# Kernel optimization log

Measured on AMD Instinct MI355X. Metric: run time of the kernel, lower is better.

## Reference

```python
import jax, jax.numpy as jnp
import numpy as np

NUM_POINTS = 2_000_000
NUM_CAMS = 200
H, W = 1080, 1920


def setup_inputs() -> dict:
    key = jax.random.key(0)
    k1, k2, k3, k4, k5, k6, k7 = jax.random.split(key, 7)
    c = jax.random.randint(k1, (NUM_POINTS,), 0, NUM_CAMS)
    y = jax.random.randint(k2, (NUM_POINTS,), 0, H)
    x = jax.random.randint(k3, (NUM_POINTS,), 0, W)
    point_indices = jnp.stack([c, y, x], axis=1)  # [N,3] int
    depth = jax.random.uniform(k4, (NUM_POINTS, 1), minval=0.1, maxval=10.0, dtype=jnp.float32)
    # nerfstudio get_image_coords(): pixel-center grid (row+0.5, col+0.5), shape [H,W,2]
    yy, xx = jnp.meshgrid(jnp.arange(H), jnp.arange(W), indexing='ij')
    image_coords = jnp.stack([yy, xx], axis=-1).astype(jnp.float32) + 0.5
    # camera_to_worlds: [C,3,4] = [R | t] with proper rotation (invertible when padded)
    Q, _ = jnp.linalg.qr(jax.random.normal(k5, (NUM_CAMS, 3, 3), dtype=jnp.float32))
    t = jax.random.normal(k6, (NUM_CAMS, 3, 1), dtype=jnp.float32) * 2.0
    camera_to_worlds = jnp.concatenate([Q, t], axis=-1)  # [C,3,4]
    # intrinsics: [C,3,3] pinhole matrices
    f = 1000.0 + 50.0 * jax.random.normal(k7, (NUM_CAMS,), dtype=jnp.float32)
    zeros = jnp.zeros_like(f)
    ones = jnp.ones_like(f)
    cx = jnp.full_like(f, W / 2.0)
    cy = jnp.full_like(f, H / 2.0)
    intrinsics = jnp.stack([
        jnp.stack([f, zeros, cx], axis=-1),
        jnp.stack([zeros, f, cy], axis=-1),
        jnp.stack([zeros, zeros, ones], axis=-1),
    ], axis=1)  # [C,3,3]
    return {
        'point_indices': point_indices,
        'depth': depth,
        'image_coords': image_coords,
        'camera_to_worlds': camera_to_worlds,
        'intrinsics': intrinsics,
    }


def reference(point_indices, depth, image_coords, camera_to_worlds, intrinsics):
    # camera_calib == 'xyz' -> no output axis permutation
    c = point_indices[:, 0]
    y = point_indices[:, 1]
    x = point_indices[:, 2]
    coords = image_coords[y, x] - 0.5  # [N,2] (row, col)
    d = depth  # [N,1]
    # X_img = [x*d, y*d, d, 1]
    X_img = jnp.concatenate([coords[:, [1, 0]] * d, d, jnp.ones_like(d)], axis=1)  # [N,4]
    # N2R = diag(1,-1,-1,1)
    n2r = jnp.diag(jnp.array([1.0, -1.0, -1.0, 1.0], dtype=jnp.float32))  # [4,4]
    E = camera_to_worlds[c]  # [N,3,4]
    bottom = jnp.broadcast_to(jnp.array([0.0, 0.0, 0.0, 1.0], dtype=jnp.float32), (E.shape[0], 1, 4))
    E_ = jnp.concatenate([E, bottom], axis=1)  # [N,4,4]
    K = intrinsics[c]  # [N,3,3]
    K_ = jnp.pad(K, ((0, 0), (0, 1), (0, 1)))  # [N,4,4] zero-padded
    K_ = K_.at[:, 3, 3].set(1.0)
    w2c = K_ @ jnp.linalg.inv(E_ @ n2r)  # [N,4,4]
    c2w = jnp.linalg.inv(w2c)
    X_world = (c2w @ X_img[..., None])[..., 0]  # [N,4]
    return X_world
```

## Files before the change

kernel.cpp:

```cpp
#include <hip/hip_runtime.h>


#define MAXCAM 256

__global__ __launch_bounds__(256) void pointgen_kernel(
    const int*   __restrict__ pi,
    const float* __restrict__ depth,
    const float* __restrict__ c2w,
    const float* __restrict__ intr,
    float4*      __restrict__ out,
    int N, int ncam)
{
    __shared__ float4 camA[MAXCAM * 3];

    for (int cam = (int)threadIdx.x; cam < ncam; cam += (int)blockDim.x) {
        const float* e = c2w  + cam * 12;
        const float* k = intr + cam * 9;
        float f  = k[0];
        float cx = k[2];
        float cy = k[5];
        float invf = 1.0f / f;
        #pragma unroll
        for (int r = 0; r < 3; ++r) {
            float R0 = e[r * 4 + 0];
            float R1 = e[r * 4 + 1];
            float R2 = e[r * 4 + 2];
            float tr = e[r * 4 + 3];
            float4 a;
            a.x = R0 * invf;
            a.y = -R1 * invf;
            a.z = (cy * R1 - cx * R0) * invf - R2;
            a.w = tr;
            camA[cam * 3 + r] = a;
        }
    }
    __syncthreads();

    int stride = (int)(gridDim.x * blockDim.x);
    for (int i = (int)(blockIdx.x * blockDim.x + threadIdx.x); i < N; i += stride) {
        int c = pi[3 * i + 0];
        int y = pi[3 * i + 1];
        int x = pi[3 * i + 2];
        float d = depth[i];
        float xd = (float)x * d;
        float yd = (float)y * d;
        float4 r0 = camA[c * 3 + 0];
        float4 r1 = camA[c * 3 + 1];
        float4 r2 = camA[c * 3 + 2];
        float4 o;
        o.x = fmaf(r0.x, xd, fmaf(r0.y, yd, fmaf(r0.z, d, r0.w)));
        o.y = fmaf(r1.x, xd, fmaf(r1.y, yd, fmaf(r1.z, d, r1.w)));
        o.z = fmaf(r2.x, xd, fmaf(r2.y, yd, fmaf(r2.z, d, r2.w)));
        o.w = 1.0f;
        out[i] = o;
    }
}

extern "C" void kernel_launch(void* const* d_in, const int* in_sizes, int n_in,
                              void* d_out, int out_size, void* d_ws, size_t ws_size,
                              hipStream_t stream) {
    const int*   pi    = (const int*)d_in[0];
    const float* depth = (const float*)d_in[1];
    const float* c2w   = (const float*)d_in[3];
    const float* intr  = (const float*)d_in[4];
    float4* out = (float4*)d_out;

    int N    = in_sizes[1];
    int ncam = in_sizes[3] / 12;
    if (ncam > MAXCAM) ncam = MAXCAM;

    int block = 256;
    int grid  = 1024;
    int max_grid = (N + block - 1) / block;
    if (grid > max_grid) grid = max_grid;

    pointgen_kernel<<<grid, block, 0, stream>>>(pi, depth, c2w, intr, out, N, ncam);
}
```

Before: 96.74 us.

## Process four points per thread with vectorized int4/float4 loads

Each thread now handles four consecutive points, reading the packed [N,3] indices as three int4 loads and the depths as one float4 load in place of scalar strided loads. The grid-stride loop is dropped for a one-shot grid sized to N/4 threads. The goal is fewer, wider memory transactions on a bandwidth-bound kernel. The cost is about 2000 blocks that each rebuild the 200-camera shared-memory table, versus 1024 before, and the wide loads assume the input buffers are 16-byte aligned.

```diff
diff --git a/kernel.cpp b/kernel.cpp
--- a/kernel.cpp
+++ b/kernel.cpp
@@ -3,7 +3,22 @@
 
 #define MAXCAM 256
 
-__global__ __launch_bounds__(256) void pointgen_kernel(
+__device__ __forceinline__ float4 proj(const float4* __restrict__ camA,
+                                       int c, int y, int x, float d) {
+    float xd = (float)x * d;
+    float yd = (float)y * d;
+    float4 r0 = camA[c * 3 + 0];
+    float4 r1 = camA[c * 3 + 1];
+    float4 r2 = camA[c * 3 + 2];
+    float4 o;
+    o.x = fmaf(r0.x, xd, fmaf(r0.y, yd, fmaf(r0.z, d, r0.w)));
+    o.y = fmaf(r1.x, xd, fmaf(r1.y, yd, fmaf(r1.z, d, r1.w)));
+    o.z = fmaf(r2.x, xd, fmaf(r2.y, yd, fmaf(r2.z, d, r2.w)));
+    o.w = 1.0f;
+    return o;
+}
+
+__global__ __launch_bounds__(256) void pointgen4_kernel(
     const int*   __restrict__ pi,
     const float* __restrict__ depth,
     const float* __restrict__ c2w,
@@ -36,23 +51,31 @@
     }
     __syncthreads();
 
-    int stride = (int)(gridDim.x * blockDim.x);
-    for (int i = (int)(blockIdx.x * blockDim.x + threadIdx.x); i < N; i += stride) {
-        int c = pi[3 * i + 0];
-        int y = pi[3 * i + 1];
-        int x = pi[3 * i + 2];
-        float d = depth[i];
-        float xd = (float)x * d;
-        float yd = (float)y * d;
-        float4 r0 = camA[c * 3 + 0];
-        float4 r1 = camA[c * 3 + 1];
-        float4 r2 = camA[c * 3 + 2];
-        float4 o;
-        o.x = fmaf(r0.x, xd, fmaf(r0.y, yd, fmaf(r0.z, d, r0.w)));
-        o.y = fmaf(r1.x, xd, fmaf(r1.y, yd, fmaf(r1.z, d, r1.w)));
-        o.z = fmaf(r2.x, xd, fmaf(r2.y, yd, fmaf(r2.z, d, r2.w)));
-        o.w = 1.0f;
-        out[i] = o;
+    int t    = (int)(blockIdx.x * blockDim.x + threadIdx.x);
+    int base = 4 * t;
+    if (base + 3 < N) {
+        const int4* pi4 = (const int4*)pi;
+        int4 w0 = pi4[3 * t + 0];
+        int4 w1 = pi4[3 * t + 1];
+        int4 w2 = pi4[3 * t + 2];
+        float4 d4 = ((const float4*)depth)[t];
+
+        float4 o0 = proj(camA, w0.x, w0.y, w0.z, d4.x);
+        float4 o1 = proj(camA, w0.w, w1.x, w1.y, d4.y);
+        float4 o2 = proj(camA, w1.z, w1.w, w2.x, d4.z);
+        float4 o3 = proj(camA, w2.y, w2.z, w2.w, d4.w);
+
+        out[base + 0] = o0;
+        out[base + 1] = o1;
+        out[base + 2] = o2;
+        out[base + 3] = o3;
+    } else if (base < N) {
+        for (int i = base; i < N; ++i) {
+            int c = pi[3 * i + 0];
+            int y = pi[3 * i + 1];
+            int x = pi[3 * i + 2];
+            out[i] = proj(camA, c, y, x, depth[i]);
+        }
     }
 }
 
@@ -69,10 +92,9 @@
     int ncam = in_sizes[3] / 12;
     if (ncam > MAXCAM) ncam = MAXCAM;
 
-    int block = 256;
-    int grid  = 1024;
-    int max_grid = (N + block - 1) / block;
-    if (grid > max_grid) grid = max_grid;
+    int block   = 256;
+    int threads = (N + 3) / 4;
+    int grid    = (threads + block - 1) / block;
 
-    pointgen_kernel<<<grid, block, 0, stream>>>(pi, depth, c2w, intr, out, N, ncam);
+    pointgen4_kernel<<<grid, block, 0, stream>>>(pi, depth, c2w, intr, out, N, ncam);
 }
```

Result: slower. 102.9 us, median of 2 (+6.3%).
